# Kernel optimization log

Hardware: AMD Instinct MI355X
Metric: run time of the kernel (lower is better)

## Reference

```python
import jax, jax.numpy as jnp
import numpy as np
from jax import lax

WINDOW_SIZE = 5
GRAD_THRESH = 0.15
MAX_ITER = 5
EPS = 1e-8


def setup_inputs() -> dict:
    key = jax.random.key(0)
    k1, k2, k3 = jax.random.split(key, 3)
    B, M, T = 16, 128, 12000
    return {
        "mel_features": jax.random.normal(k1, (B, M, T), jnp.float32),
        "spectral_features": jax.random.normal(k2, (B, T), jnp.float32),
        "initial_boundaries": jax.random.uniform(k3, (B, T), dtype=jnp.float32),
        "similarity_weights": jnp.ones(3, jnp.float32) / 3.0,
    }


def _consistency_scores(mel, spec, weights):
    # mel: (B, M, T), spec: (B, T), weights: (3,)
    B, M, T = mel.shape
    # cosine similarity between consecutive frames (vectorized over t)
    a, b = mel[:, :, :-1], mel[:, :, 1:]
    dot = jnp.sum(a * b, axis=1)
    na = jnp.sqrt(jnp.sum(a * a, axis=1))
    nb = jnp.sqrt(jnp.sum(b * b, axis=1))
    cos = dot / (jnp.maximum(na, EPS) * jnp.maximum(nb, EPS))  # (B, T-1)
    mel_sim = jnp.pad(cos, ((0, 0), (1, 0)))  # t=0 stays 0 (torch init zeros)

    spec_diff = jnp.abs(spec[:, 1:] - spec[:, :-1])
    spec_sim = jnp.pad(1.0 / (1.0 + spec_diff), ((0, 0), (1, 0)), constant_values=1.0)

    # avg_pool1d(mean over mel bins, k, stride=1, pad=k//2, count_include_pad)
    k = min(WINDOW_SIZE, T)
    mean_mel = jnp.mean(mel, axis=1)  # (B, T)
    pad = k // 2
    padded = jnp.pad(mean_mel, ((0, 0), (pad, pad)))
    cs = jnp.pad(jnp.cumsum(padded, axis=1), ((0, 0), (1, 0)))
    smooth = (cs[:, k:] - cs[:, :-k]) / k  # (B, T)
    # torch.std default is unbiased (ddof=1)
    temporal = 1.0 - jnp.std(smooth, axis=1, ddof=1, keepdims=True)  # (B, 1)
    temporal = jnp.broadcast_to(temporal, (B, T))

    return weights[0] * mel_sim + weights[1] * spec_sim + weights[2] * temporal


def _adjustments(candidates, cons):
    # local mean of cons over [t-2, t+3) clipped to [0, T)
    B, T = cons.shape
    cs = jnp.pad(jnp.cumsum(cons, axis=1), ((0, 0), (1, 0)))  # (B, T+1)
    t = jnp.arange(T)
    lo = jnp.maximum(t - 2, 0)
    hi = jnp.minimum(t + 3, T)
    local = (cs[:, hi] - cs[:, lo]) / (hi - lo).astype(cons.dtype)
    interior = (t >= 1) & (t <= T - 2)  # loop ran over range(1, T-1)
    active = (candidates > 0.5) & interior
    return jnp.where(active & (local > 0.7), -0.1,
                     jnp.where(active & (local < 0.4), 0.1, 0.0)).astype(cons.dtype)


def reference(mel_features, spectral_features, initial_boundaries, similarity_weights):
    weights = jax.nn.softmax(similarity_weights)
    cons = _consistency_scores(mel_features, spectral_features, weights)
    # gradient-based candidates are fixed across iterations (cons is fixed)
    grads = jnp.pad(jnp.abs(cons[:, 1:] - cons[:, :-1]), ((0, 0), (1, 0)))
    cand_static = (grads > GRAD_THRESH).astype(cons.dtype)

    def body(carry, _):
        refined, done = carry
        candidates = jnp.maximum(cand_static, refined)
        adj = _adjustments(candidates, cons)
        adj = jnp.where(done, 0.0, adj)  # replicate early break by freezing
        new_refined = jnp.clip(refined + adj, 0.0, 1.0)
        new_done = done | (jnp.sum(jnp.abs(adj)) < 0.01)
        return (new_refined, new_done), None

    (refined, _), _ = lax.scan(body, (initial_boundaries, jnp.array(False)),
                               None, length=MAX_ITER)
    return refined
```

## Files before the change

### kernel.cpp

```cpp
#include <hip/hip_runtime.h>
#include <cstdint>

#define BB 16
#define MM 128
#define TT 12000
constexpr int BT = BB * TT;


__global__ void k1_colstats(const float* __restrict__ mel,
                            float* __restrict__ ssq,
                            float* __restrict__ dotv,
                            float* __restrict__ cmean,
                            unsigned int* __restrict__ counts) {
    if (blockIdx.x == 0 && blockIdx.y == 0 && threadIdx.x < 8)
        counts[threadIdx.x] = 0u;
    const int b = blockIdx.y;
    const int t = blockIdx.x * blockDim.x + threadIdx.x;
    if (t >= TT) return;
    const float* base = mel + (size_t)b * MM * TT;
    float accd = 0.f, accq = 0.f, accs = 0.f;
    {
#pragma clang fp contract(off)
        for (int m = 0; m < MM; ++m) {
            const float* rowp = base + (size_t)m * TT;
            float cur = rowp[t];
            float prev = (t > 0) ? rowp[t - 1] : 0.f;
            accd += prev * cur;
            accq += cur * cur;
            accs += cur;
        }
    }
    size_t i = (size_t)b * TT + t;
    ssq[i] = accq; dotv[i] = accd; cmean[i] = accs * (1.0f / MM);
}

__global__ void kA_temporal(const float* __restrict__ cmean,
                            float* __restrict__ temporal) {
    const int b = blockIdx.x;
    const int tid = threadIdx.x;
    __shared__ __align__(16) float row_s[TT];
    __shared__ float red[256];
    __shared__ float mean_s;
    const float4* c4 = (const float4*)(cmean + (size_t)b * TT);
    float4* r4 = (float4*)row_s;
    for (int i = tid; i < TT / 4; i += 256) r4[i] = c4[i];
    __syncthreads();

    float s = 0.f;
    for (int t = tid; t < TT; t += 256) {
        float v = 0.f;
        int lo = t - 2 < 0 ? 0 : t - 2;
        int hi = t + 2 >= TT ? TT - 1 : t + 2;
        for (int j = lo; j <= hi; ++j) v += row_s[j];
        s += v / 5.0f;
    }
    red[tid] = s; __syncthreads();
    for (int o = 128; o > 0; o >>= 1) {
        if (tid < o) red[tid] += red[tid + o];
        __syncthreads();
    }
    if (tid == 0) mean_s = red[0] / (float)TT;
    __syncthreads();
    float mean = mean_s;
    float ss = 0.f;
    for (int t = tid; t < TT; t += 256) {
        float v = 0.f;
        int lo = t - 2 < 0 ? 0 : t - 2;
        int hi = t + 2 >= TT ? TT - 1 : t + 2;
        for (int j = lo; j <= hi; ++j) v += row_s[j];
        float sm = v / 5.0f - mean;
        ss += sm * sm;
    }
    red[tid] = ss; __syncthreads();
    for (int o = 128; o > 0; o >>= 1) {
        if (tid < o) red[tid] += red[tid + o];
        __syncthreads();
    }
    if (tid == 0) {
        float var = red[0] / (float)(TT - 1);
        temporal[b] = 1.0f - sqrtf(var);
    }
}

__global__ void kB_cons(const float* __restrict__ ssq,
                        const float* __restrict__ dotv,
                        const float* __restrict__ spec,
                        const float* __restrict__ temporal,
                        const float* __restrict__ wraw,
                        float* __restrict__ cons,
                        float* __restrict__ consq) {
    const int idx = blockIdx.x * 256 + threadIdx.x;
    const int b = idx / TT;
    const int t = idx - b * TT;
    float x0 = wraw[0], x1 = wraw[1], x2 = wraw[2];
    float mx = fmaxf(x0, fmaxf(x1, x2));
    float e0 = expf(x0 - mx), e1 = expf(x1 - mx), e2 = expf(x2 - mx);
    float es = (e0 + e1) + e2;
    float w0 = e0 / es, w1 = e1 / es, w2 = e2 / es;
    float mel_sim, spec_sim;
    if (t == 0) { mel_sim = 0.f; spec_sim = 1.f; }
    else {
        float na = fmaxf(sqrtf(ssq[idx - 1]), 1e-8f);
        float nb = fmaxf(sqrtf(ssq[idx]),     1e-8f);
        float den = na * nb; asm volatile("" : "+v"(den));
        mel_sim = dotv[idx] / den;
        float d = fabsf(spec[idx] - spec[idx - 1]);
        spec_sim = 1.0f / (1.0f + d);
    }
    float pa = w0 * mel_sim;     asm volatile("" : "+v"(pa));
    float pb = w1 * spec_sim;    asm volatile("" : "+v"(pb));
    float pc = w2 * temporal[b]; asm volatile("" : "+v"(pc));
    float c = (pa + pb) + pc;
    cons[idx] = c;
    consq[((t >> 2) * 16 + b) * 4 + (t & 3)] = c;
}

#define QCH(P, a, b, c, d) \
    "v_add_f32 v" a ", v" P ", v" a "\n\t" \
    "v_add_f32 v" b ", v" a ", v" b "\n\t" \
    "v_add_f32 v" c ", v" b ", v" c "\n\t" \
    "v_add_f32 v" d ", v" c ", v" d "\n\t"

#define SB8(a0,a1,a2,a3, b0,b1,b2,b3, c0,c1,c2,c3, d0,d1,d2,d3, \
            e0,e1,e2,e3, f0,f1,f2,f3, g0,g1,g2,g3, h0,h1,h2,h3) \
    "s_waitcnt vmcnt(48)\n\t" \
    QCH("43", a0, a1, a2, a3) \
    QCH(a3,   b0, b1, b2, b3) \
    QCH(b3,   c0, c1, c2, c3) \
    QCH(c3,   d0, d1, d2, d3) \
    QCH(d3,   e0, e1, e2, e3) \
    QCH(e3,   f0, f1, f2, f3) \
    QCH(f3,   g0, g1, g2, g3) \
    QCH(g3,   h0, h1, h2, h3) \
    "v_mov_b32 v43, v" h3 "\n\t" \
    "global_store_dwordx4 v40, v[" a0 ":" a3 "], %1 offset:0\n\t" \
    "global_store_dwordx4 v40, v[" b0 ":" b3 "], %1 offset:256\n\t" \
    "global_store_dwordx4 v40, v[" c0 ":" c3 "], %1 offset:512\n\t" \
    "global_store_dwordx4 v40, v[" d0 ":" d3 "], %1 offset:768\n\t" \
    "global_store_dwordx4 v40, v[" e0 ":" e3 "], %1 offset:1024\n\t" \
    "global_store_dwordx4 v40, v[" f0 ":" f3 "], %1 offset:1280\n\t" \
    "global_store_dwordx4 v40, v[" g0 ":" g3 "], %1 offset:1536\n\t" \
    "global_store_dwordx4 v40, v[" h0 ":" h3 "], %1 offset:1792\n\t" \
    "global_load_dwordx4 v[" a0 ":" a3 "], v42, %0 offset:0\n\t" \
    "global_load_dwordx4 v[" b0 ":" b3 "], v42, %0 offset:256\n\t" \
    "global_load_dwordx4 v[" c0 ":" c3 "], v42, %0 offset:512\n\t" \
    "global_load_dwordx4 v[" d0 ":" d3 "], v42, %0 offset:768\n\t" \
    "global_load_dwordx4 v[" e0 ":" e3 "], v42, %0 offset:1024\n\t" \
    "global_load_dwordx4 v[" f0 ":" f3 "], v42, %0 offset:1280\n\t" \
    "global_load_dwordx4 v[" g0 ":" g3 "], v42, %0 offset:1536\n\t" \
    "global_load_dwordx4 v[" h0 ":" h3 "], v42, %0 offset:1792\n\t" \
    "v_add_u32 v40, 0x800, v40\n\t" \
    "v_add_u32 v42, 0x800, v42\n\t"

#define PRO8(a0,a1,a2,a3, b0,b1,b2,b3, c0,c1,c2,c3, d0,d1,d2,d3, \
             e0,e1,e2,e3, f0,f1,f2,f3, g0,g1,g2,g3, h0,h1,h2,h3) \
    "global_load_dwordx4 v[" a0 ":" a3 "], v42, %0 offset:0\n\t" \
    "global_load_dwordx4 v[" b0 ":" b3 "], v42, %0 offset:256\n\t" \
    "global_load_dwordx4 v[" c0 ":" c3 "], v42, %0 offset:512\n\t" \
    "global_load_dwordx4 v[" d0 ":" d3 "], v42, %0 offset:768\n\t" \
    "global_load_dwordx4 v[" e0 ":" e3 "], v42, %0 offset:1024\n\t" \
    "global_load_dwordx4 v[" f0 ":" f3 "], v42, %0 offset:1280\n\t" \
    "global_load_dwordx4 v[" g0 ":" g3 "], v42, %0 offset:1536\n\t" \
    "global_load_dwordx4 v[" h0 ":" h3 "], v42, %0 offset:1792\n\t" \
    "v_add_u32 v42, 0x800, v42\n\t"

#define BNA "48","49","50","51","52","53","54","55","56","57","58","59","60","61","62","63","64","65","66","67","68","69","70","71","72","73","74","75","76","77","78","79"
#define BNB "80","81","82","83","84","85","86","87","88","89","90","91","92","93","94","95","96","97","98","99","100","101","102","103","104","105","106","107","108","109","110","111"
#define BNC "112","113","114","115","116","117","118","119","120","121","122","123","124","125","126","127","128","129","130","131","132","133","134","135","136","137","138","139","140","141","142","143"
#define BND "144","145","146","147","148","149","150","151","152","153","154","155","156","157","158","159","160","161","162","163","164","165","166","167","168","169","170","171","172","173","174","175"
#define XP(M, ...) M(__VA_ARGS__)

__global__ void __launch_bounds__(256)
kC_scan16(const float* __restrict__ consq,
          float* __restrict__ CSq) {
    const int tid = threadIdx.x;
    if (tid >= 64) {
        const float4* s4 = (const float4*)consq;
        const int lane = tid - 64;
        for (int it = 0; it < 32; ++it) {
            float4 tmp[8];
#pragma unroll
            for (int i = 0; i < 8; ++i)
                tmp[i] = s4[(size_t)it * 1536 + lane + 192 * i];
#pragma unroll
            for (int i = 0; i < 8; ++i)
                asm volatile("" :: "v"(tmp[i].x), "v"(tmp[i].y),
                                   "v"(tmp[i].z), "v"(tmp[i].w));
        }
        return;
    }
    const int r = tid;
    if (r >= BB) return;
    uint32_t voff = (uint32_t)(r * 16);
    asm volatile(
        "v_mov_b32 v40, %2\n\t"
        "v_mov_b32 v42, %2\n\t"
        "v_mov_b32 v43, 0\n\t"
        XP(PRO8, BNA)
        XP(PRO8, BNB)
        XP(PRO8, BNC)
        XP(PRO8, BND)
        "s_waitcnt vmcnt(0)\n\t"
        "s_mov_b32 s20, 94\n\t"
        "3:\n\t"
        XP(SB8, BNA)
        XP(SB8, BNB)
        XP(SB8, BNC)
        XP(SB8, BND)
        "s_sub_u32 s20, s20, 1\n\t"
        "s_cmp_lg_u32 s20, 0\n\t"
        "s_cbranch_scc1 3b\n\t"
        "s_waitcnt vmcnt(0)\n\t"
        :
        : "s"(consq), "s"(CSq), "v"(voff)
        : "v40", "v42", "v43",
          "v48","v49","v50","v51","v52","v53","v54","v55",
          "v56","v57","v58","v59","v60","v61","v62","v63",
          "v64","v65","v66","v67","v68","v69","v70","v71",
          "v72","v73","v74","v75","v76","v77","v78","v79",
          "v80","v81","v82","v83","v84","v85","v86","v87",
          "v88","v89","v90","v91","v92","v93","v94","v95",
          "v96","v97","v98","v99","v100","v101","v102","v103",
          "v104","v105","v106","v107","v108","v109","v110","v111",
          "v112","v113","v114","v115","v116","v117","v118","v119",
          "v120","v121","v122","v123","v124","v125","v126","v127",
          "v128","v129","v130","v131","v132","v133","v134","v135",
          "v136","v137","v138","v139","v140","v141","v142","v143",
          "v144","v145","v146","v147","v148","v149","v150","v151",
          "v152","v153","v154","v155","v156","v157","v158","v159",
          "v160","v161","v162","v163","v164","v165","v166","v167",
          "v168","v169","v170","v171","v172","v173","v174","v175",
          "s20", "scc", "memory");
}

__global__ void kD_flags(const float* __restrict__ cons,
                         const float* __restrict__ CSq,
                         const float* __restrict__ init,
                         unsigned int* __restrict__ counts) {
    const int idx = blockIdx.x * 256 + threadIdx.x;
    const int b = idx / TT;
    const int t = idx - b * TT;
    __shared__ unsigned sflag[5];
    if (threadIdx.x < 5) sflag[threadIdx.x] = 0u;
    __syncthreads();

    int lo = t - 2; if (lo < 0) lo = 0;
    int hi = t + 3; if (hi > TT) hi = TT;
    int uh = hi - 1;
    float csH = CSq[((uh >> 2) * 16 + b) * 4 + (uh & 3)];
    float csL = 0.f;
    if (lo > 0) {
        int ul = lo - 1;
        csL = CSq[((ul >> 2) * 16 + b) * 4 + (ul & 3)];
    }
    float local = (csH - csL) / (float)(hi - lo);
    float dir = (local > 0.7f) ? -0.1f : ((local < 0.4f) ? 0.1f : 0.0f);
    bool interior = (t >= 1) && (t <= TT - 2);
    float step = interior ? dir : 0.0f;
    float g = (t == 0) ? 0.f : fabsf(cons[idx] - cons[idx - 1]);
    float cand = (g > 0.15f) ? 1.f : 0.f;
    float r = init[idx];
    bool nz[5];
#pragma unroll
    for (int j = 0; j < 5; ++j) {
        float adj = (fmaxf(cand, r) > 0.5f) ? step : 0.0f;
        nz[j] = (adj != 0.0f);
        r = fminf(fmaxf(r + adj, 0.0f), 1.0f);
    }
    const int lane = threadIdx.x & 63;
#pragma unroll
    for (int j = 0; j < 5; ++j) {
        unsigned long long mb = __ballot(nz[j]);
        if (lane == 0 && mb) atomicOr(&sflag[j], 1u);
    }
    __syncthreads();
    if (threadIdx.x < 5 && sflag[threadIdx.x]) counts[threadIdx.x] = 1u;
}

__global__ void k_final(const float* __restrict__ cons,
                        const float* __restrict__ CSq,
                        const float* __restrict__ init,
                        const unsigned int* __restrict__ counts,
                        float* __restrict__ outp) {
    const int idx = blockIdx.x * 256 + threadIdx.x;
    const int b = idx / TT;
    const int t = idx - b * TT;

    int lo = t - 2; if (lo < 0) lo = 0;
    int hi = t + 3; if (hi > TT) hi = TT;
    int uh = hi - 1;
    float csH = CSq[((uh >> 2) * 16 + b) * 4 + (uh & 3)];
    float csL = 0.f;
    if (lo > 0) {
        int ul = lo - 1;
        csL = CSq[((ul >> 2) * 16 + b) * 4 + (ul & 3)];
    }
    float local = (csH - csL) / (float)(hi - lo);
    float dir = (local > 0.7f) ? -0.1f : ((local < 0.4f) ? 0.1f : 0.0f);
    bool interior = (t >= 1) && (t <= TT - 2);
    float step = interior ? dir : 0.0f;
    float g = (t == 0) ? 0.f : fabsf(cons[idx] - cons[idx - 1]);
    float cand = (g > 0.15f) ? 1.f : 0.f;

    float r = init[idx];
    unsigned c[5];
#pragma unroll
    for (int j = 0; j < 5; ++j) c[j] = counts[j];
#pragma unroll
    for (int j = 0; j < 5; ++j) {
        if (c[j] == 0u) break;
        float adj = (fmaxf(cand, r) > 0.5f) ? step : 0.0f;
        r = fminf(fmaxf(r + adj, 0.0f), 1.0f);
    }
    outp[idx] = r;
}

extern "C" void kernel_launch(void* const* d_in, const int* in_sizes, int n_in,
                              void* d_out, int out_size, void* d_ws, size_t ws_size,
                              hipStream_t stream) {
    const float* mel  = (const float*)d_in[0];
    const float* spec = (const float*)d_in[1];
    const float* init = (const float*)d_in[2];
    const float* wts  = (const float*)d_in[3];

    float* ws = (float*)d_ws;
    float* ssq   = ws;
    float* dotv  = ws + 192000;
    float* cmean = ws + 384000;
    float* cons  = ws + 576000;
    float* consq = ws + 768000;
    float* CSq   = ws + 962560;
    float* temporal = ws + 1157120;
    unsigned int* counts = (unsigned int*)(ws + 1157136);

    dim3 g1((TT + 255) / 256, BB);
    k1_colstats<<<g1, 256, 0, stream>>>(mel, ssq, dotv, cmean, counts);
    kA_temporal<<<BB, 256, 0, stream>>>(cmean, temporal);
    kB_cons<<<BT / 256, 256, 0, stream>>>(ssq, dotv, spec, temporal, wts, cons, consq);
    kC_scan16<<<1, 256, 0, stream>>>(consq, CSq);
    kD_flags<<<BT / 256, 256, 0, stream>>>(cons, CSq, init, counts);
    k_final<<<BT / 256, 256, 0, stream>>>(cons, CSq, init, counts, (float*)d_out);
}
```

Measured before the change: 123.1 us.

## Widen serial scan to full wavefront using ds_bpermute redistribution

The single-block sequential prefix scan previously used 16 lanes, one per batch row, each walking a long chain of float4 loads. It now uses all 64 lanes of the wavefront to load wider chunks and redistributes them with ds_bpermute, so each batch lane processes several quad groups per iteration. This cuts the loop trip count and register footprint. The costs are cross-lane permute latency and extra lgkmcnt waits on the serial add chain, and the workspace offsets are enlarged, with some lanes writing a second half-buffer.

```diff
diff --git a/kernel.cpp b/kernel.cpp
--- a/kernel.cpp
+++ b/kernel.cpp
@@ -121,53 +121,71 @@
     "v_add_f32 v" c ", v" b ", v" c "\n\t" \
     "v_add_f32 v" d ", v" c ", v" d "\n\t"
 
-#define SB8(a0,a1,a2,a3, b0,b1,b2,b3, c0,c1,c2,c3, d0,d1,d2,d3, \
-            e0,e1,e2,e3, f0,f1,f2,f3, g0,g1,g2,g3, h0,h1,h2,h3) \
-    "s_waitcnt vmcnt(48)\n\t" \
-    QCH("43", a0, a1, a2, a3) \
-    QCH(a3,   b0, b1, b2, b3) \
-    QCH(b3,   c0, c1, c2, c3) \
-    QCH(c3,   d0, d1, d2, d3) \
-    QCH(d3,   e0, e1, e2, e3) \
-    QCH(e3,   f0, f1, f2, f3) \
-    QCH(f3,   g0, g1, g2, g3) \
-    QCH(g3,   h0, h1, h2, h3) \
-    "v_mov_b32 v43, v" h3 "\n\t" \
-    "global_store_dwordx4 v40, v[" a0 ":" a3 "], %1 offset:0\n\t" \
-    "global_store_dwordx4 v40, v[" b0 ":" b3 "], %1 offset:256\n\t" \
-    "global_store_dwordx4 v40, v[" c0 ":" c3 "], %1 offset:512\n\t" \
-    "global_store_dwordx4 v40, v[" d0 ":" d3 "], %1 offset:768\n\t" \
-    "global_store_dwordx4 v40, v[" e0 ":" e3 "], %1 offset:1024\n\t" \
-    "global_store_dwordx4 v40, v[" f0 ":" f3 "], %1 offset:1280\n\t" \
-    "global_store_dwordx4 v40, v[" g0 ":" g3 "], %1 offset:1536\n\t" \
-    "global_store_dwordx4 v40, v[" h0 ":" h3 "], %1 offset:1792\n\t" \
-    "global_load_dwordx4 v[" a0 ":" a3 "], v42, %0 offset:0\n\t" \
-    "global_load_dwordx4 v[" b0 ":" b3 "], v42, %0 offset:256\n\t" \
-    "global_load_dwordx4 v[" c0 ":" c3 "], v42, %0 offset:512\n\t" \
-    "global_load_dwordx4 v[" d0 ":" d3 "], v42, %0 offset:768\n\t" \
-    "global_load_dwordx4 v[" e0 ":" e3 "], v42, %0 offset:1024\n\t" \
-    "global_load_dwordx4 v[" f0 ":" f3 "], v42, %0 offset:1280\n\t" \
-    "global_load_dwordx4 v[" g0 ":" g3 "], v42, %0 offset:1536\n\t" \
-    "global_load_dwordx4 v[" h0 ":" h3 "], v42, %0 offset:1792\n\t" \
+#define SBW(QA0,QA1,QA2,QA3, QB0,QB1,QB2,QB3) \
+    "s_waitcnt vmcnt(50)\n\t" \
+    "ds_bpermute_b32 v96,  %4, v" QA0 "\n\t" \
+    "ds_bpermute_b32 v97,  %4, v" QA1 "\n\t" \
+    "ds_bpermute_b32 v98,  %4, v" QA2 "\n\t" \
+    "ds_bpermute_b32 v99,  %4, v" QA3 "\n\t" \
+    "ds_bpermute_b32 v100, %5, v" QA0 "\n\t" \
+    "ds_bpermute_b32 v101, %5, v" QA1 "\n\t" \
+    "ds_bpermute_b32 v102, %5, v" QA2 "\n\t" \
+    "ds_bpermute_b32 v103, %5, v" QA3 "\n\t" \
+    "ds_bpermute_b32 v104, %6, v" QA0 "\n\t" \
+    "ds_bpermute_b32 v105, %6, v" QA1 "\n\t" \
+    "ds_bpermute_b32 v106, %6, v" QA2 "\n\t" \
+    "ds_bpermute_b32 v107, %6, v" QA3 "\n\t" \
+    QCH("43", QA0, QA1, QA2, QA3) \
+    "s_waitcnt lgkmcnt(8)\n\t" \
+    QCH(QA3, "96", "97", "98", "99") \
+    "s_waitcnt lgkmcnt(4)\n\t" \
+    QCH("99", "100", "101", "102", "103") \
+    "s_waitcnt lgkmcnt(0)\n\t" \
+    QCH("103", "104", "105", "106", "107") \
+    "ds_bpermute_b32 v108, %4, v" QB0 "\n\t" \
+    "ds_bpermute_b32 v109, %4, v" QB1 "\n\t" \
+    "ds_bpermute_b32 v110, %4, v" QB2 "\n\t" \
+    "ds_bpermute_b32 v111, %4, v" QB3 "\n\t" \
+    "ds_bpermute_b32 v112, %5, v" QB0 "\n\t" \
+    "ds_bpermute_b32 v113, %5, v" QB1 "\n\t" \
+    "ds_bpermute_b32 v114, %5, v" QB2 "\n\t" \
+    "ds_bpermute_b32 v115, %5, v" QB3 "\n\t" \
+    "ds_bpermute_b32 v116, %6, v" QB0 "\n\t" \
+    "ds_bpermute_b32 v117, %6, v" QB1 "\n\t" \
+    "ds_bpermute_b32 v118, %6, v" QB2 "\n\t" \
+    "ds_bpermute_b32 v119, %6, v" QB3 "\n\t" \
+    QCH("107", QB0, QB1, QB2, QB3) \
+    "s_waitcnt lgkmcnt(8)\n\t" \
+    QCH(QB3, "108", "109", "110", "111") \
+    "s_waitcnt lgkmcnt(4)\n\t" \
+    QCH("111", "112", "113", "114", "115") \
+    "s_waitcnt lgkmcnt(0)\n\t" \
+    QCH("115", "116", "117", "118", "119") \
+    "v_mov_b32 v43, v119\n\t" \
+    "global_store_dwordx4 v40, v[" QA0 ":" QA3 "], %1 offset:0\n\t" \
+    "global_store_dwordx4 v40, v[96:99],   %1 offset:256\n\t" \
+    "global_store_dwordx4 v40, v[100:103], %1 offset:512\n\t" \
+    "global_store_dwordx4 v40, v[104:107], %1 offset:768\n\t" \
+    "global_store_dwordx4 v40, v[" QB0 ":" QB3 "], %1 offset:1024\n\t" \
+    "global_store_dwordx4 v40, v[108:111], %1 offset:1280\n\t" \
+    "global_store_dwordx4 v40, v[112:115], %1 offset:1536\n\t" \
+    "global_store_dwordx4 v40, v[116:119], %1 offset:1792\n\t" \
+    "global_load_dwordx4 v[" QA0 ":" QA3 "], v42, %0 offset:0\n\t" \
+    "global_load_dwordx4 v[" QB0 ":" QB3 "], v42, %0 offset:1024\n\t" \
     "v_add_u32 v40, 0x800, v40\n\t" \
     "v_add_u32 v42, 0x800, v42\n\t"
 
-#define PRO8(a0,a1,a2,a3, b0,b1,b2,b3, c0,c1,c2,c3, d0,d1,d2,d3, \
-             e0,e1,e2,e3, f0,f1,f2,f3, g0,g1,g2,g3, h0,h1,h2,h3) \
-    "global_load_dwordx4 v[" a0 ":" a3 "], v42, %0 offset:0\n\t" \
-    "global_load_dwordx4 v[" b0 ":" b3 "], v42, %0 offset:256\n\t" \
-    "global_load_dwordx4 v[" c0 ":" c3 "], v42, %0 offset:512\n\t" \
-    "global_load_dwordx4 v[" d0 ":" d3 "], v42, %0 offset:768\n\t" \
-    "global_load_dwordx4 v[" e0 ":" e3 "], v42, %0 offset:1024\n\t" \
-    "global_load_dwordx4 v[" f0 ":" f3 "], v42, %0 offset:1280\n\t" \
-    "global_load_dwordx4 v[" g0 ":" g3 "], v42, %0 offset:1536\n\t" \
-    "global_load_dwordx4 v[" h0 ":" h3 "], v42, %0 offset:1792\n\t" \
+#define PROW(QA0,QA1,QA2,QA3, QB0,QB1,QB2,QB3) \
+    "global_load_dwordx4 v[" QA0 ":" QA3 "], v42, %0 offset:0\n\t" \
+    "global_load_dwordx4 v[" QB0 ":" QB3 "], v42, %0 offset:1024\n\t" \
     "v_add_u32 v42, 0x800, v42\n\t"
 
-#define BNA "48","49","50","51","52","53","54","55","56","57","58","59","60","61","62","63","64","65","66","67","68","69","70","71","72","73","74","75","76","77","78","79"
-#define BNB "80","81","82","83","84","85","86","87","88","89","90","91","92","93","94","95","96","97","98","99","100","101","102","103","104","105","106","107","108","109","110","111"
-#define BNC "112","113","114","115","116","117","118","119","120","121","122","123","124","125","126","127","128","129","130","131","132","133","134","135","136","137","138","139","140","141","142","143"
-#define BND "144","145","146","147","148","149","150","151","152","153","154","155","156","157","158","159","160","161","162","163","164","165","166","167","168","169","170","171","172","173","174","175"
+#define S0 "48","49","50","51","52","53","54","55"
+#define S1 "56","57","58","59","60","61","62","63"
+#define S2 "64","65","66","67","68","69","70","71"
+#define S3 "72","73","74","75","76","77","78","79"
+#define S4 "80","81","82","83","84","85","86","87"
+#define S5 "88","89","90","91","92","93","94","95"
 #define XP(M, ...) M(__VA_ARGS__)
 
 __global__ void __launch_bounds__(256)
@@ -189,30 +207,34 @@
         }
         return;
     }
-    const int r = tid;
-    if (r >= BB) return;
-    uint32_t voff = (uint32_t)(r * 16);
+    uint32_t lvoff = (uint32_t)(tid * 16);
+    uint32_t svoff = (uint32_t)(((tid >> 4) ? 786432u : 0u)
+                                + (tid & 15) * 16);
+    uint32_t a1 = (uint32_t)(((tid & 15) + 16) * 4);
+    uint32_t a2 = (uint32_t)(((tid & 15) + 32) * 4);
+    uint32_t a3 = (uint32_t)(((tid & 15) + 48) * 4);
     asm volatile(
-        "v_mov_b32 v40, %2\n\t"
+        "v_mov_b32 v40, %3\n\t"
         "v_mov_b32 v42, %2\n\t"
         "v_mov_b32 v43, 0\n\t"
-        XP(PRO8, BNA)
-        XP(PRO8, BNB)
-        XP(PRO8, BNC)
-        XP(PRO8, BND)
+        XP(PROW, S0) XP(PROW, S1) XP(PROW, S2)
+        XP(PROW, S3) XP(PROW, S4) XP(PROW, S5)
         "s_waitcnt vmcnt(0)\n\t"
-        "s_mov_b32 s20, 94\n\t"
+        "s_mov_b32 s20, 63\n\t"
         "3:\n\t"
-        XP(SB8, BNA)
-        XP(SB8, BNB)
-        XP(SB8, BNC)
-        XP(SB8, BND)
+        XP(SBW, S0)
+        XP(SBW, S1)
+        XP(SBW, S2)
+        XP(SBW, S3)
+        XP(SBW, S4)
+        XP(SBW, S5)
         "s_sub_u32 s20, s20, 1\n\t"
         "s_cmp_lg_u32 s20, 0\n\t"
         "s_cbranch_scc1 3b\n\t"
-        "s_waitcnt vmcnt(0)\n\t"
+        "s_waitcnt vmcnt(0) lgkmcnt(0)\n\t"
         :
-        : "s"(consq), "s"(CSq), "v"(voff)
+        : "s"(consq), "s"(CSq), "v"(lvoff), "v"(svoff),
+          "v"(a1), "v"(a2), "v"(a3)
         : "v40", "v42", "v43",
           "v48","v49","v50","v51","v52","v53","v54","v55",
           "v56","v57","v58","v59","v60","v61","v62","v63",
@@ -223,13 +245,6 @@
           "v96","v97","v98","v99","v100","v101","v102","v103",
           "v104","v105","v106","v107","v108","v109","v110","v111",
           "v112","v113","v114","v115","v116","v117","v118","v119",
-          "v120","v121","v122","v123","v124","v125","v126","v127",
-          "v128","v129","v130","v131","v132","v133","v134","v135",
-          "v136","v137","v138","v139","v140","v141","v142","v143",
-          "v144","v145","v146","v147","v148","v149","v150","v151",
-          "v152","v153","v154","v155","v156","v157","v158","v159",
-          "v160","v161","v162","v163","v164","v165","v166","v167",
-          "v168","v169","v170","v171","v172","v173","v174","v175",
           "s20", "scc", "memory");
 }
 
@@ -329,9 +344,9 @@
     float* cmean = ws + 384000;
     float* cons  = ws + 576000;
     float* consq = ws + 768000;
-    float* CSq   = ws + 962560;
-    float* temporal = ws + 1157120;
-    unsigned int* counts = (unsigned int*)(ws + 1157136);
+    float* CSq   = ws + 964608;
+    float* temporal = ws + 1357824;
+    unsigned int* counts = (unsigned int*)(ws + 1357840);
 
     dim3 g1((TT + 255) / 256, BB);
     k1_colstats<<<g1, 256, 0, stream>>>(mel, ssq, dotv, cmean, counts);
```

New measurement: 148.5 us. +20.6%, slower.
